# Kernel tuning notes

Hardware: AMD Instinct MI355X
Metric: run time of the kernel (lower is better)

The kernel has to match this reference:

```python
import jax, jax.numpy as jnp
import numpy as np

B, T, D, U, C = 256, 512, 128, 128, 64


def setup_inputs() -> dict:
    key = jax.random.key(0)
    ks = jax.random.split(key, 4)
    s_in = 1.0 / np.sqrt(D)
    s_u = 1.0 / np.sqrt(U)
    return {
        "inputs": jax.random.normal(ks[0], (B, T, D), dtype=jnp.float32),
        "W1": jax.random.normal(ks[1], (D, U), dtype=jnp.float32) * s_in,
        "b1": jnp.zeros((U,), dtype=jnp.float32),
        "W2": jax.random.normal(ks[2], (U, U), dtype=jnp.float32) * s_u,
        "b2": jnp.zeros((U,), dtype=jnp.float32),
        "Wc": jax.random.normal(ks[3], (U, C), dtype=jnp.float32) * s_u,
        "bc": jnp.zeros((C,), dtype=jnp.float32),
    }


def reference(inputs, W1, b1, W2, b2, Wc, bc):
    # state_{t} = tanh(x_t @ W1 + b1) + tanh(state_{t-1} @ W2 + b2)
    # Input projection has no recurrent dependency -> precompute in one big GEMM.
    h = jnp.tanh(jnp.einsum("btd,du->btu", inputs, W1) + b1)  # (B, T, U)

    def step(state, h_t):
        y = h_t + jnp.tanh(state @ W2 + b2)  # (B, U)
        return y, y

    state0 = jnp.zeros((inputs.shape[0], W2.shape[0]), dtype=inputs.dtype)
    _, ys = jax.lax.scan(step, state0, jnp.swapaxes(h, 0, 1))  # ys: (T, B, U)
    features = jnp.swapaxes(ys, 0, 1)  # (B, T, U)
    # classifier: Dense head applied to stacked features
    return jnp.einsum("btu,uc->btc", features, Wc) + bc
```

## Files before the change

kernel.cpp:

```cpp
#include <hip/hip_runtime.h>

#define NB 256
#define NT 512
#define ND 128
#define NU 128
#define NC 64
#define NM (NB * NT)
#define YP 136
#define SCL 2.8853900817779268f

typedef _Float16 half2v __attribute__((ext_vector_type(2)));
typedef _Float16 half4v __attribute__((ext_vector_type(4)));
typedef _Float16 half8v __attribute__((ext_vector_type(8)));
typedef float f32x4 __attribute__((ext_vector_type(4)));
typedef float v2f __attribute__((ext_vector_type(2)));

#define MFMA(a, b, c) __builtin_amdgcn_mfma_f32_16x16x32_f16((a), (b), (c), 0, 0, 0)

__device__ __forceinline__ half2v pk2(float a, float b) {
  return __builtin_bit_cast(half2v, __builtin_amdgcn_cvt_pkrtz(a, b));
}

__device__ __forceinline__ float tanh_s(float s) {
  float e = __builtin_amdgcn_exp2f(s);
  return fmaf(-2.0f, __builtin_amdgcn_rcpf(e + 1.0f), 1.0f);
}
__device__ __forceinline__ float ym1(float s, float th) {
  float e = __builtin_amdgcn_exp2f(s);
  return fmaf(-2.0f, __builtin_amdgcn_rcpf(e + 1.0f), th);
}

__device__ __forceinline__ void wg_barrier() {
  asm volatile("s_waitcnt lgkmcnt(0)\n\ts_barrier" ::: "memory");
}

__global__ __launch_bounds__(256, 1) void k1_inproj(
    const float* __restrict__ x, const float* __restrict__ W1,
    const float* __restrict__ b1v, _Float16* __restrict__ TH)
{
  __shared__ _Float16 W1T[ND * YP];
  const int tid = (int)threadIdx.x;
  for (int i = tid; i < ND * NU / 2; i += 256) {
    int n = i & 127, kh = i >> 7;
    half2v p = {(_Float16)(SCL * W1[(size_t)(2 * kh) * NU + n]),
                (_Float16)(SCL * W1[(size_t)(2 * kh + 1) * NU + n])};
    *(half2v*)&W1T[n * YP + 2 * kh] = p;
  }
  __syncthreads();

  const int L = tid & 63, wv = tid >> 6;
  const int v = L & 15, q = L >> 4;
  const int m0 = (int)blockIdx.x * 64 + wv * 16;

  const float* xr = x + (size_t)(m0 + v) * ND + 8 * q;
  half8v xf[4];
#pragma unroll
  for (int kk = 0; kk < 4; ++kk) {
    float4 a = *(const float4*)(xr + 32 * kk);
    float4 b = *(const float4*)(xr + 32 * kk + 4);
    half2v p0 = pk2(a.x, a.y), p1 = pk2(a.z, a.w);
    half2v p2 = pk2(b.x, b.y), p3 = pk2(b.z, b.w);
    xf[kk] = (half8v){p0[0], p0[1], p1[0], p1[1], p2[0], p2[1], p3[0], p3[1]};
  }

#pragma unroll
  for (int ht = 0; ht < 8; ++ht) {
    f32x4 acc;
    {
      float4 bb = *(const float4*)&b1v[16 * ht + 4 * q];
      acc = (f32x4){SCL * bb.x, SCL * bb.y, SCL * bb.z, SCL * bb.w};
    }
#pragma unroll
    for (int kk = 0; kk < 4; ++kk) {
      half8v wa = *(const half8v*)&W1T[(16 * ht + v) * YP + 32 * kk + 8 * q];
      acc = MFMA(wa, xf[kk], acc);
    }
    half2v zlo = pk2(tanh_s(acc[0]), tanh_s(acc[1]));
    half2v zhi = pk2(tanh_s(acc[2]), tanh_s(acc[3]));
    half4v z = {zlo[0], zlo[1], zhi[0], zhi[1]};
    *(half4v*)&TH[(size_t)(m0 + v) * NU + 16 * ht + 4 * q] = z;
  }
}

__global__ __launch_bounds__(640, 1) void k2_recur(
    const _Float16* __restrict__ TH, const float* __restrict__ W2,
    const float* __restrict__ b2v, const float* __restrict__ Wc,
    const float* __restrict__ bcv, float* __restrict__ out)
{
  __shared__ _Float16 Ybuf[2][16 * YP];

  const int tid = (int)threadIdx.x;
  const int w = tid >> 6;
  const int L = tid & 63;
  const int v = L & 15, q = L >> 4;
  const int b0 = (int)blockIdx.x * 16;
  const _Float16* rd = &Ybuf[0][0] + v * YP + 8 * q;
  const f32x4 zero4 = (f32x4){0.f, 0.f, 0.f, 0.f};

  if (w < 8) {
    half8v w2f[4];
#pragma unroll
    for (int kk = 0; kk < 4; ++kk) {
      half8v h;
#pragma unroll
      for (int j = 0; j < 8; ++j)
        h[j] = (_Float16)(SCL * W2[(size_t)(32 * kk + 8 * q + j) * NU + 16 * w + v]);
      w2f[kk] = h;
    }
    f32x4 racc, b2f;
    {
      const int h0 = 16 * w + 4 * q;
      float4 bb = *(const float4*)&b2v[h0];
      racc = (f32x4){SCL * bb.x, SCL * bb.y, SCL * bb.z, SCL * bb.w};
      f32x4 cs = zero4;
#pragma unroll 4
      for (int k = 0; k < NU; ++k) {
        float4 ww = *(const float4*)&W2[(size_t)k * NU + h0];
        cs += (f32x4){ww.x, ww.y, ww.z, ww.w};
      }
      b2f = racc + (f32x4){SCL * cs[0], SCL * cs[1], SCL * cs[2], SCL * cs[3]};
    }

    const _Float16* thp = TH + ((size_t)(b0 + v) * NT) * NU + 16 * w + 4 * q;
    _Float16* wr = &Ybuf[0][0] + v * YP + 16 * w + 4 * q;

    half4v thr0 = *(const half4v*)(thp + 0 * NU);
    half4v thr1 = *(const half4v*)(thp + 1 * NU);
    half4v thr2 = *(const half4v*)(thp + 2 * NU);
    half4v thr3 = *(const half4v*)(thp + 3 * NU);

#define RSTEP(T_, THR_, BUF_)                                                 \
  {                                                                           \
    half2v ylo = pk2(ym1(racc[0], (float)THR_[0]),                            \
                     ym1(racc[1], (float)THR_[1]));                           \
    half2v yhi = pk2(ym1(racc[2], (float)THR_[2]),                            \
                     ym1(racc[3], (float)THR_[3]));                           \
    half4v y4 = {ylo[0], ylo[1], yhi[0], yhi[1]};                             \
    *(half4v*)(wr + (BUF_) * (16 * YP)) = y4;                                 \
    {                                                                         \
      int tn = (T_) + 4; tn = tn < NT ? tn : NT - 1;                          \
      THR_ = *(const half4v*)(thp + (size_t)tn * NU);                         \
    }                                                                         \
    wg_barrier();                                                             \
    {                                                                         \
      half8v yf0 = *(const half8v*)(rd + (BUF_) * (16 * YP) + 0);             \
      half8v yf1 = *(const half8v*)(rd + (BUF_) * (16 * YP) + 32);            \
      half8v yf2 = *(const half8v*)(rd + (BUF_) * (16 * YP) + 64);            \
      half8v yf3 = *(const half8v*)(rd + (BUF_) * (16 * YP) + 96);            \
      f32x4 ra = MFMA(w2f[0], yf0, b2f);        \
      f32x4 rb = MFMA(w2f[1], yf1, zero4);                                    \
      ra = MFMA(w2f[2], yf2, ra);                                             \
      rb = MFMA(w2f[3], yf3, rb);                                             \
      racc = ra + rb;                                                         \
    }                                                                         \
  }

#pragma unroll 1
    for (int t = 0; t < NT; t += 4) {
      RSTEP(t + 0, thr0, 0)
      RSTEP(t + 1, thr1, 1)
      RSTEP(t + 2, thr2, 0)
      RSTEP(t + 3, thr3, 1)
    }
#undef RSTEP
  } else {
    const int hw = w - 8;
    half8v wcf[2][4];
    f32x4 bcf[2];
#pragma unroll
    for (int c2 = 0; c2 < 2; ++c2) {
      const int ct = 2 * hw + c2;
#pragma unroll
      for (int kk = 0; kk < 4; ++kk) {
        half8v h;
#pragma unroll
        for (int j = 0; j < 8; ++j)
          h[j] = (_Float16)Wc[(size_t)(32 * kk + 8 * q + j) * NC + 16 * ct + v];
        wcf[c2][kk] = h;
      }
      const int c0 = 16 * ct + 4 * q;
      float4 bb = *(const float4*)&bcv[c0];
      f32x4 cs = zero4;
#pragma unroll 4
      for (int k = 0; k < NU; ++k) {
        float4 ww = *(const float4*)&Wc[(size_t)k * NC + c0];
        cs += (f32x4){ww.x, ww.y, ww.z, ww.w};
      }
      bcf[c2] = cs + (f32x4){bb.x, bb.y, bb.z, bb.w};
    }
    float* op = out + ((size_t)(b0 + v) * NT) * NC + 4 * q;

#define HSTEP(T_, BUF_)                                                       \
  {                                                                           \
    wg_barrier();                                                             \
    half8v yf0 = *(const half8v*)(rd + (BUF_) * (16 * YP) + 0);               \
    half8v yf1 = *(const half8v*)(rd + (BUF_) * (16 * YP) + 32);              \
    half8v yf2 = *(const half8v*)(rd + (BUF_) * (16 * YP) + 64);              \
    half8v yf3 = *(const half8v*)(rd + (BUF_) * (16 * YP) + 96);              \
    _Pragma("unroll")                                                         \
    for (int c2 = 0; c2 < 2; ++c2) {                                          \
      f32x4 oa = MFMA(wcf[c2][0], yf0, bcf[c2]);                              \
      f32x4 ob = MFMA(wcf[c2][1], yf1, zero4);                                \
      oa = MFMA(wcf[c2][2], yf2, oa);                                         \
      ob = MFMA(wcf[c2][3], yf3, ob);                                         \
      f32x4 oo = oa + ob;                                                     \
      *(float4*)(op + (size_t)(T_) * NC + 16 * (2 * hw + c2)) =               \
          (float4){oo[0], oo[1], oo[2], oo[3]};                               \
    }                                                                         \
  }

#pragma unroll 1
    for (int t = 0; t < NT; t += 2) {
      HSTEP(t + 0, 0)
      HSTEP(t + 1, 1)
    }
#undef HSTEP
  }
}

__device__ __forceinline__ float fast_tanh(float x) {
  float e = __expf(2.0f * x);
  return 1.0f - 2.0f / (e + 1.0f);
}
__device__ __forceinline__ float bcast(float val, int i) {
  return __builtin_bit_cast(float, __builtin_amdgcn_readlane(__builtin_bit_cast(int, val), i));
}

__global__ __launch_bounds__(256, 1) void rnn_fallback(
    const float* __restrict__ x, const float* __restrict__ W1,
    const float* __restrict__ b1v, const float* __restrict__ W2,
    const float* __restrict__ b2v, const float* __restrict__ Wc,
    const float* __restrict__ bcv, float* __restrict__ out)
{
  __shared__ float xring[16][ND];
  __shared__ float pH[2][4][NU];
  __shared__ float pR[2][4][NU];
  __shared__ float pC[2][4][NC];

  const int tid  = (int)threadIdx.x;
  const int lane = tid & 63;
  const int kg   = tid >> 6;
  const int b    = (int)blockIdx.x;
  const float4* xr4 = (const float4*)(x + (size_t)b * NT * ND);

  v2f w1f[32], w2f[32];
  float wcf[32];
#pragma unroll
  for (int i = 0; i < 32; ++i) {
    int k = kg * 32 + i;
    w1f[i] = (v2f){W1[k * NU + lane], W1[k * NU + lane + 64]};
    w2f[i] = (v2f){W2[k * NU + lane], W2[k * NU + lane + 64]};
    wcf[i] = Wc[k * NC + lane];
  }
  const float biasc = bcv[lane];
  float bias1 = 0.f, bias2 = 0.f;
  if (lane < 32) { bias1 = b1v[kg * 32 + lane]; bias2 = b2v[kg * 32 + lane]; }

  float4 stg = make_float4(0.f, 0.f, 0.f, 0.f);
  if (lane < 32) {
    float4 a0 = xr4[(kg + 0) * 32 + lane];
    float4 a1 = xr4[(kg + 4) * 32 + lane];
    ((float4*)xring[kg + 0])[lane] = a0;
    ((float4*)xring[kg + 4])[lane] = a1;
    stg = xr4[(kg + 8) * 32 + lane];
  }
  float yseg = 0.f;
  wg_barrier();

  for (int t = 0; t < NT; ++t) {
    const int pb = t & 1;
    v2f accH0 = {0.f, 0.f}, accH1 = {0.f, 0.f};
    const float4* xb = (const float4*)&xring[t & 15][kg * 32];
#pragma unroll
    for (int i = 0; i < 4; ++i) {
      float4 xa = xb[2 * i];
      float4 xc = xb[2 * i + 1];
      accH0 = w1f[8*i+0] * (v2f){xa.x, xa.x} + accH0;
      accH1 = w1f[8*i+1] * (v2f){xa.y, xa.y} + accH1;
      accH0 = w1f[8*i+2] * (v2f){xa.z, xa.z} + accH0;
      accH1 = w1f[8*i+3] * (v2f){xa.w, xa.w} + accH1;
      accH0 = w1f[8*i+4] * (v2f){xc.x, xc.x} + accH0;
      accH1 = w1f[8*i+5] * (v2f){xc.y, xc.y} + accH1;
      accH0 = w1f[8*i+6] * (v2f){xc.z, xc.z} + accH0;
      accH1 = w1f[8*i+7] * (v2f){xc.w, xc.w} + accH1;
    }
    v2f accH = accH0 + accH1;
    v2f accR0 = {0.f, 0.f}, accR1 = {0.f, 0.f};
    float accC0 = 0.f, accC1 = 0.f;
#pragma unroll
    for (int i = 0; i < 16; ++i) {
      float s0 = bcast(yseg, 2 * i);
      float s1 = bcast(yseg, 2 * i + 1);
      accR0 = w2f[2*i+0] * (v2f){s0, s0} + accR0;
      accR1 = w2f[2*i+1] * (v2f){s1, s1} + accR1;
      accC0 = fmaf(s0, wcf[2*i+0], accC0);
      accC1 = fmaf(s1, wcf[2*i+1], accC1);
    }
    v2f accR = accR0 + accR1;
    float accC = accC0 + accC1;

    pH[pb][kg][lane]      = accH.x;
    pH[pb][kg][lane + 64] = accH.y;
    pR[pb][kg][lane]      = accR.x;
    pR[pb][kg][lane + 64] = accR.y;
    pC[pb][kg][lane]      = accC;

    if (kg == (t & 3)) {
      if (lane < 32) {
        ((float4*)xring[(t + 8) & 15])[lane] = stg;
        int r = t + 12; r = (r < NT) ? r : (NT - 1);
        stg = xr4[r * 32 + lane];
      }
    }
    wg_barrier();
    if (lane < 32) {
      const int j = kg * 32 + lane;
      float hs = bias1, rs = bias2;
#pragma unroll
      for (int g = 0; g < 4; ++g) { hs += pH[pb][g][j]; rs += pR[pb][g][j]; }
      yseg = fast_tanh(hs) + fast_tanh(rs);
    }
    if (kg == ((t + 2) & 3) && t >= 1) {
      float cs = biasc;
#pragma unroll
      for (int g = 0; g < 4; ++g) cs += pC[pb][g][lane];
      out[((size_t)b * NT + (t - 1)) * NC + lane] = cs;
    }
  }
  float accC0 = 0.f, accC1 = 0.f;
#pragma unroll
  for (int i = 0; i < 16; ++i) {
    float s0 = bcast(yseg, 2 * i);
    float s1 = bcast(yseg, 2 * i + 1);
    accC0 = fmaf(s0, wcf[2*i+0], accC0);
    accC1 = fmaf(s1, wcf[2*i+1], accC1);
  }
  pC[0][kg][lane] = accC0 + accC1;
  wg_barrier();
  if (kg == 0) {
    float cs = biasc;
#pragma unroll
    for (int g = 0; g < 4; ++g) cs += pC[0][g][lane];
    out[((size_t)b * NT + (NT - 1)) * NC + lane] = cs;
  }
}

extern "C" void kernel_launch(void* const* d_in, const int* in_sizes, int n_in,
                              void* d_out, int out_size, void* d_ws, size_t ws_size,
                              hipStream_t stream) {
  (void)in_sizes; (void)n_in; (void)out_size;
  const float* x   = (const float*)d_in[0];
  const float* W1  = (const float*)d_in[1];
  const float* b1v = (const float*)d_in[2];
  const float* W2  = (const float*)d_in[3];
  const float* b2v = (const float*)d_in[4];
  const float* Wc  = (const float*)d_in[5];
  const float* bcv = (const float*)d_in[6];
  float* out = (float*)d_out;

  const size_t need = (size_t)NM * NU * 2;
  if (ws_size >= need) {
    _Float16* TH = (_Float16*)d_ws;
    hipLaunchKernelGGL(k1_inproj, dim3(NM / 64), dim3(256), 0, stream, x, W1, b1v, TH);
    hipLaunchKernelGGL(k2_recur, dim3(NB / 16), dim3(640), 0, stream,
                       TH, W2, b2v, Wc, bcv, out);
  } else {
    hipLaunchKernelGGL(rnn_fallback, dim3(NB), dim3(256), 0, stream,
                       x, W1, b1v, W2, b2v, Wc, bcv, out);
  }
}
```

Before: 303.5 us.

## Swizzle recurrent Y buffer layout, raise recurrence priority, software-pipeline head reads

Replaces the padded row layout of the shared Y double buffer with a fragment-ordered layout, so each lane reads its MFMA operand as one contiguous 8-half chunk without bank conflicts. It also raises the scheduling priority of the recurrence waves. The head waves now load Y for step t right after the barrier and compute the output for step t-1 in the next iteration, which keeps their LDS reads off the barrier path. The risk is that the writers' address mapping must exactly match the new fragment order, and the deferred head compute relies on double-buffer timing remaining correct.

```diff
diff --git a/kernel.cpp b/kernel.cpp
--- a/kernel.cpp
+++ b/kernel.cpp
@@ -87,14 +87,14 @@
     const float* __restrict__ b2v, const float* __restrict__ Wc,
     const float* __restrict__ bcv, float* __restrict__ out)
 {
-  __shared__ _Float16 Ybuf[2][16 * YP];
+  __shared__ _Float16 Ybuf[2][2048];
 
   const int tid = (int)threadIdx.x;
   const int w = tid >> 6;
   const int L = tid & 63;
   const int v = L & 15, q = L >> 4;
   const int b0 = (int)blockIdx.x * 16;
-  const _Float16* rd = &Ybuf[0][0] + v * YP + 8 * q;
+  const _Float16* rd = &Ybuf[0][0] + L * 8;
   const f32x4 zero4 = (f32x4){0.f, 0.f, 0.f, 0.f};
 
   if (w < 8) {
@@ -122,12 +122,15 @@
     }
 
     const _Float16* thp = TH + ((size_t)(b0 + v) * NT) * NU + 16 * w + 4 * q;
-    _Float16* wr = &Ybuf[0][0] + v * YP + 16 * w + 4 * q;
+    _Float16* wr = &Ybuf[0][0] + (w >> 1) * 512 +
+                   (v + 16 * (2 * (w & 1) + (q >> 1))) * 8 + 4 * (q & 1);
 
     half4v thr0 = *(const half4v*)(thp + 0 * NU);
     half4v thr1 = *(const half4v*)(thp + 1 * NU);
     half4v thr2 = *(const half4v*)(thp + 2 * NU);
     half4v thr3 = *(const half4v*)(thp + 3 * NU);
+
+    __builtin_amdgcn_s_setprio(1);
 
 #define RSTEP(T_, THR_, BUF_)                                                 \
   {                                                                           \
@@ -136,17 +139,17 @@
     half2v yhi = pk2(ym1(racc[2], (float)THR_[2]),                            \
                      ym1(racc[3], (float)THR_[3]));                           \
     half4v y4 = {ylo[0], ylo[1], yhi[0], yhi[1]};                             \
-    *(half4v*)(wr + (BUF_) * (16 * YP)) = y4;                                 \
+    *(half4v*)(wr + (BUF_) * 2048) = y4;                                      \
     {                                                                         \
       int tn = (T_) + 4; tn = tn < NT ? tn : NT - 1;                          \
       THR_ = *(const half4v*)(thp + (size_t)tn * NU);                         \
     }                                                                         \
     wg_barrier();                                                             \
     {                                                                         \
-      half8v yf0 = *(const half8v*)(rd + (BUF_) * (16 * YP) + 0);             \
-      half8v yf1 = *(const half8v*)(rd + (BUF_) * (16 * YP) + 32);            \
-      half8v yf2 = *(const half8v*)(rd + (BUF_) * (16 * YP) + 64);            \
-      half8v yf3 = *(const half8v*)(rd + (BUF_) * (16 * YP) + 96);            \
+      half8v yf0 = *(const half8v*)(rd + (BUF_) * 2048 + 0);                  \
+      half8v yf1 = *(const half8v*)(rd + (BUF_) * 2048 + 512);                \
+      half8v yf2 = *(const half8v*)(rd + (BUF_) * 2048 + 1024);               \
+      half8v yf3 = *(const half8v*)(rd + (BUF_) * 2048 + 1536);               \
       f32x4 ra = MFMA(w2f[0], yf0, b2f);        \
       f32x4 rb = MFMA(w2f[1], yf1, zero4);                                    \
       ra = MFMA(w2f[2], yf2, ra);                                             \
@@ -188,33 +191,41 @@
       }
       bcf[c2] = cs + (f32x4){bb.x, bb.y, bb.z, bb.w};
     }
-    float* op = out + ((size_t)(b0 + v) * NT) * NC + 4 * q;
-
-#define HSTEP(T_, BUF_)                                                       \
-  {                                                                           \
-    wg_barrier();                                                             \
-    half8v yf0 = *(const half8v*)(rd + (BUF_) * (16 * YP) + 0);               \
-    half8v yf1 = *(const half8v*)(rd + (BUF_) * (16 * YP) + 32);              \
-    half8v yf2 = *(const half8v*)(rd + (BUF_) * (16 * YP) + 64);              \
-    half8v yf3 = *(const half8v*)(rd + (BUF_) * (16 * YP) + 96);              \
-    _Pragma("unroll")                                                         \
-    for (int c2 = 0; c2 < 2; ++c2) {                                          \
-      f32x4 oa = MFMA(wcf[c2][0], yf0, bcf[c2]);                              \
-      f32x4 ob = MFMA(wcf[c2][1], yf1, zero4);                                \
-      oa = MFMA(wcf[c2][2], yf2, oa);                                         \
-      ob = MFMA(wcf[c2][3], yf3, ob);                                         \
-      f32x4 oo = oa + ob;                                                     \
-      *(float4*)(op + (size_t)(T_) * NC + 16 * (2 * hw + c2)) =               \
-          (float4){oo[0], oo[1], oo[2], oo[3]};                               \
-    }                                                                         \
-  }
-
+    float* op = out + ((size_t)(b0 + v) * NT) * NC + 4 * q + 32 * hw;
+
+    half8v pf0, pf1, pf2, pf3;
 #pragma unroll 1
-    for (int t = 0; t < NT; t += 2) {
-      HSTEP(t + 0, 0)
-      HSTEP(t + 1, 1)
-    }
-#undef HSTEP
+    for (int t = 0; t < NT; ++t) {
+      wg_barrier();
+      if (t > 0) {
+#pragma unroll
+        for (int c2 = 0; c2 < 2; ++c2) {
+          f32x4 oa = MFMA(wcf[c2][0], pf0, bcf[c2]);
+          f32x4 ob = MFMA(wcf[c2][1], pf1, zero4);
+          oa = MFMA(wcf[c2][2], pf2, oa);
+          ob = MFMA(wcf[c2][3], pf3, ob);
+          f32x4 oo = oa + ob;
+          *(float4*)(op + (size_t)(t - 1) * NC + 16 * c2) =
+              (float4){oo[0], oo[1], oo[2], oo[3]};
+        }
+      }
+      const _Float16* rb = rd + (t & 1) * 2048;
+      pf0 = *(const half8v*)(rb + 0);
+      pf1 = *(const half8v*)(rb + 512);
+      pf2 = *(const half8v*)(rb + 1024);
+      pf3 = *(const half8v*)(rb + 1536);
+    }
+    asm volatile("s_waitcnt lgkmcnt(0)" ::: "memory");
+#pragma unroll
+    for (int c2 = 0; c2 < 2; ++c2) {
+      f32x4 oa = MFMA(wcf[c2][0], pf0, bcf[c2]);
+      f32x4 ob = MFMA(wcf[c2][1], pf1, zero4);
+      oa = MFMA(wcf[c2][2], pf2, oa);
+      ob = MFMA(wcf[c2][3], pf3, ob);
+      f32x4 oo = oa + ob;
+      *(float4*)(op + (size_t)(NT - 1) * NC + 16 * c2) =
+          (float4){oo[0], oo[1], oo[2], oo[3]};
+    }
   }
 }
 
```

Measured after the change: 302.3 us. About the same (-0.4%).
